# Kernel tuning notes

Hardware: AMD Instinct MI355X
Metric: run time of the kernel (lower is better)

The kernel has to match this reference:

```python
import jax, jax.numpy as jnp
import numpy as np

H = 2048          # hidden_size
NH = 32           # num_attention_heads
NKV = 8           # num_key_value_heads
HD = H // NH      # head_dim = 64
ROT = int(HD * 0.25)  # rotary_ndims = 16
THETA = 10000.0


def _rope_cos_sin(seq_len, position_ids):
    # inv_freq over the rotary dims
    inv_freq = 1.0 / (THETA ** (jnp.arange(0, ROT, 2, dtype=jnp.float32) / ROT))
    t = jnp.arange(seq_len, dtype=jnp.float32)
    freqs = jnp.outer(t, inv_freq)              # [S, ROT/2]
    emb = jnp.concatenate([freqs, freqs], -1)   # [S, ROT]
    cos = jnp.cos(emb)[position_ids][:, None]   # [B, 1, Q, ROT]
    sin = jnp.sin(emb)[position_ids][:, None]
    return cos, sin


def _rotate_half(x):
    x1, x2 = jnp.split(x, 2, axis=-1)
    return jnp.concatenate([-x2, x1], axis=-1)


def setup_inputs() -> dict:
    key = jax.random.key(0)
    ks = jax.random.split(key, 5)
    B, S = 2, 2048
    hidden_states = jax.random.normal(ks[0], (B, S, H), jnp.float32)
    # additive causal mask
    neg = jnp.finfo(jnp.float32).min
    causal = jnp.where(jnp.tril(jnp.ones((S, S), bool)), 0.0, neg).astype(jnp.float32)
    attention_mask = jnp.broadcast_to(causal[None, None], (B, 1, S, S))
    position_ids = jnp.broadcast_to(jnp.arange(S, dtype=jnp.int32)[None], (B, S))
    sc = 0.02
    Wq = jax.random.normal(ks[1], (H, H), jnp.float32) * sc
    Wk = jax.random.normal(ks[2], (NKV * HD, H), jnp.float32) * sc
    Wv = jax.random.normal(ks[3], (NKV * HD, H), jnp.float32) * sc
    Wo = jax.random.normal(ks[4], (H, H), jnp.float32) * sc
    return {"hidden_states": hidden_states, "attention_mask": attention_mask,
            "position_ids": position_ids, "Wq": Wq, "Wk": Wk, "Wv": Wv, "Wo": Wo}


def reference(hidden_states, attention_mask, position_ids, Wq, Wk, Wv, Wo):
    B, S, _ = hidden_states.shape
    q = (hidden_states @ Wq.T).reshape(B, S, NH, HD).transpose(0, 2, 1, 3)    # [B,NH,S,HD]
    k = (hidden_states @ Wk.T).reshape(B, S, NKV, HD).transpose(0, 2, 1, 3)   # [B,NKV,S,HD]
    v = (hidden_states @ Wv.T).reshape(B, S, NKV, HD).transpose(0, 2, 1, 3)

    cos, sin = _rope_cos_sin(S, position_ids)  # [B,1,S,ROT]
    q_rot, q_pass = q[..., :ROT], q[..., ROT:]
    k_rot, k_pass = k[..., :ROT], k[..., ROT:]
    q_rot = q_rot * cos + _rotate_half(q_rot) * sin
    k_rot = k_rot * cos + _rotate_half(k_rot) * sin
    q = jnp.concatenate([q_rot, q_pass], -1)
    k = jnp.concatenate([k_rot, k_pass], -1)

    # GQA without materializing repeated K/V: group Q heads per KV head
    G = NH // NKV
    qg = q.reshape(B, NKV, G, S, HD)
    scores = jnp.einsum('bhgqd,bhkd->bhgqk', qg, k) / np.sqrt(HD)
    scores = scores.reshape(B, NH, S, S) + attention_mask
    probs = jax.nn.softmax(scores.astype(jnp.float32), axis=-1).astype(q.dtype)
    out = jnp.einsum('bhgqk,bhkd->bhgqd', probs.reshape(B, NKV, G, S, S), v)
    out = out.reshape(B, NH, S, HD).transpose(0, 2, 1, 3).reshape(B, S, H)
    return out @ Wo.T
```

## Files before the change

kernel.cpp:

```cpp
#include <hip/hip_runtime.h>

typedef unsigned short u16;
typedef short s16x8 __attribute__((ext_vector_type(8)));
typedef u16 u16x8 __attribute__((ext_vector_type(8)));
typedef float f32x4 __attribute__((ext_vector_type(4)));
typedef __bf16 bf16x8 __attribute__((ext_vector_type(8)));

#define B_ 2
#define S_ 2048
#define H_ 2048
#define NH_ 32
#define NKV_ 8
#define HD_ 64
#define LDQ_ 3072
#define NTOK (B_ * S_)

__device__ __forceinline__ u16 f2bf(float f) {
  unsigned u = __float_as_uint(f);
  u += 0x7fffu + ((u >> 16) & 1u);
  return (u16)(u >> 16);
}
__device__ __forceinline__ float bf2f(u16 h) {
  return __uint_as_float(((unsigned)h) << 16);
}

__device__ __forceinline__ void gload16(const void* g, void* l) {
  __builtin_amdgcn_global_load_lds(
      (const __attribute__((address_space(1))) unsigned int*)g,
      (__attribute__((address_space(3))) unsigned int*)l, 16, 0, 0);
}

__device__ __forceinline__ f32x4 mfma16(s16x8 a, s16x8 b, f32x4 c) {
  return __builtin_amdgcn_mfma_f32_16x16x32_bf16(
      __builtin_bit_cast(bf16x8, a), __builtin_bit_cast(bf16x8, b), c, 0, 0, 0);
}

__global__ __launch_bounds__(256) void cvt_all(const float* __restrict__ hs,
    const float* __restrict__ wq, const float* __restrict__ wk,
    const float* __restrict__ wv, const float* __restrict__ wo,
    u16* __restrict__ xbf, u16* __restrict__ wqkv, u16* __restrict__ wob) {
  int i = blockIdx.x * 256 + threadIdx.x;
  const float* s; u16* d; int j;
  if (i < 1048576)      { s = hs; d = xbf;            j = i; }
  else if (i < 1572864) { s = wq; d = wqkv;           j = i - 1048576; }
  else if (i < 1703936) { s = wk; d = wqkv + 4194304; j = i - 1572864; }
  else if (i < 1835008) { s = wv; d = wqkv + 5242880; j = i - 1703936; }
  else                  { s = wo; d = wob;            j = i - 1835008; }
  const float4* sp = (const float4*)s + (size_t)j * 2;
  float4 a = sp[0], b = sp[1];
  u16x8 o;
  o[0] = f2bf(a.x); o[1] = f2bf(a.y); o[2] = f2bf(a.z); o[3] = f2bf(a.w);
  o[4] = f2bf(b.x); o[5] = f2bf(b.y); o[6] = f2bf(b.z); o[7] = f2bf(b.w);
  *((u16x8*)d + j) = o;
}

__global__ __launch_bounds__(256) void rope_table(float* __restrict__ tab) {
  int i = blockIdx.x * 256 + threadIdx.x;
  if (i >= S_ * 8) return;
  int p = i >> 3, k = i & 7;
  float inv = powf(10000.0f, -(float)k * 0.125f);
  float ang = (float)p * inv;
  tab[p * 16 + k] = cosf(ang);
  tab[p * 16 + 8 + k] = sinf(ang);
}

__global__ __launch_bounds__(256) void rope_apply(u16* __restrict__ C,
                                                  const int* __restrict__ pos,
                                                  const float* __restrict__ tab) {
  int t = blockIdx.x * 256 + threadIdx.x;
  if (t >= NTOK * 40) return;
  int token = t / 40, hh = t - token * 40;
  u16* p = C + (size_t)token * LDQ_ + (hh < 32 ? hh * 64 : 2048 + (hh - 32) * 64);
  const float* ct = tab + (size_t)pos[token] * 16;
  float x[16];
#pragma unroll
  for (int i = 0; i < 16; ++i) x[i] = bf2f(p[i]);
#pragma unroll
  for (int i = 0; i < 8; ++i) {
    float c = ct[i], s = ct[8 + i];
    p[i]     = f2bf(x[i] * c - x[i + 8] * s);
    p[i + 8] = f2bf(x[i + 8] * c + x[i] * s);
  }
}

__global__ __launch_bounds__(256) void vtrans(const u16* __restrict__ C,
                                              u16* __restrict__ Vt) {
  __shared__ u16 tile[64][72];
  int st = blockIdx.x;
  int kv = blockIdx.y;
  int tid = threadIdx.x;
  const u16* src = C + ((size_t)(kv >> 3) * S_ + (size_t)st * 64) * LDQ_ + 2560 + (kv & 7) * 64;
#pragma unroll
  for (int it = 0; it < 2; ++it) {
    int c = it * 256 + tid;
    int s = c >> 3, d0 = (c & 7) * 8;
    *(u16x8*)&tile[s][d0] = *(const u16x8*)(src + (size_t)s * LDQ_ + d0);
  }
  __syncthreads();
  u16* dst = Vt + (size_t)kv * HD_ * S_ + st * 64;
  int s = tid & 63;
#pragma unroll
  for (int it = 0; it < 16; ++it) {
    int d = it * 4 + (tid >> 6);
    dst[(size_t)d * S_ + s] = tile[s][d];
  }
}

__device__ __forceinline__ void store_c(u16* p, float v) { *p = f2bf(v); }
__device__ __forceinline__ void store_c(float* p, float v) { *p = v; }

template <typename OutT>
__global__ __launch_bounds__(256, 3) void gemm_bt(const u16* __restrict__ A,
                                                  const u16* __restrict__ Bw,
                                                  OutT* __restrict__ C,
                                                  int M, int N, int K) {
  __shared__ u16 lds[2 * 128 * 64];
  u16* ldsA = lds;
  u16* ldsB = lds + 128 * 64;
  const int tid = threadIdx.x;
  const int lane = tid & 63;
  const int wave = tid >> 6;
  const int wm = (wave & 1) * 64;
  const int wn = (wave >> 1) * 64;
  const int m0 = blockIdx.y * 128;
  const int n0 = blockIdx.x * 128;
  const int l15 = lane & 15;
  const int quad = lane >> 4;

  f32x4 acc[4][4];
#pragma unroll
  for (int i = 0; i < 4; ++i)
#pragma unroll
    for (int j = 0; j < 4; ++j) acc[i][j] = {0.f, 0.f, 0.f, 0.f};

  const u16* Ab = A + (size_t)m0 * K;
  const u16* Bb = Bw + (size_t)n0 * K;

  for (int k0 = 0; k0 < K; k0 += 64) {
    __syncthreads();
#pragma unroll
    for (int it = 0; it < 4; ++it) {
      int c = it * 256 + tid;
      int row = c >> 3;
      int kk = (c & 7) * 8;
      gload16(Ab + (size_t)row * K + k0 + kk, ldsA + (size_t)c * 8);
      gload16(Bb + (size_t)row * K + k0 + kk, ldsB + (size_t)c * 8);
    }
    __syncthreads();
#pragma unroll
    for (int ks = 0; ks < 2; ++ks) {
      int ko = ks * 32 + quad * 8;
      s16x8 af[4], bfr[4];
#pragma unroll
      for (int i = 0; i < 4; ++i)
        af[i] = *(const s16x8*)(ldsA + (size_t)(wm + i * 16 + l15) * 64 + ko);
#pragma unroll
      for (int j = 0; j < 4; ++j)
        bfr[j] = *(const s16x8*)(ldsB + (size_t)(wn + j * 16 + l15) * 64 + ko);
#pragma unroll
      for (int i = 0; i < 4; ++i)
#pragma unroll
        for (int j = 0; j < 4; ++j)
          acc[i][j] = mfma16(af[i], bfr[j], acc[i][j]);
    }
  }
#pragma unroll
  for (int i = 0; i < 4; ++i) {
    int row = m0 + wm + i * 16 + quad * 4;
#pragma unroll
    for (int j = 0; j < 4; ++j) {
      int col = n0 + wn + j * 16 + l15;
#pragma unroll
      for (int r = 0; r < 4; ++r) store_c(C + (size_t)(row + r) * N + col, acc[i][j][r]);
    }
  }
}

#define KSTRIDE 72
#define PSTRIDE 72
#define SC_ 0.18033688011112042f
#define M0_ 4.0f

template <bool DIAG>
__device__ __forceinline__ void softmax_pack(const f32x4* sc, f32x4& lacc,
                                             u16* pwq, int sb, int qg) {
#pragma unroll
  for (int nt = 0; nt < 4; ++nt) {
    f32x4 p;
#pragma unroll
    for (int r = 0; r < 4; ++r) {
      float v = fmaf(sc[nt][r], SC_, -M0_);
      float e = __builtin_amdgcn_exp2f(v);
      if (DIAG) e = (sb + nt * 16 + r > qg) ? 0.0f : e;
      p[r] = e;
    }
    lacc += p;
    unsigned lo = __builtin_amdgcn_perm(__float_as_uint(p[1]) + 0x8000u,
                                        __float_as_uint(p[0]) + 0x8000u,
                                        0x07060302u);
    unsigned hi = __builtin_amdgcn_perm(__float_as_uint(p[3]) + 0x8000u,
                                        __float_as_uint(p[2]) + 0x8000u,
                                        0x07060302u);
    *(unsigned*)(pwq + nt * 16) = lo;
    *(unsigned*)(pwq + nt * 16 + 2) = hi;
  }
}

__global__ __launch_bounds__(256, 3) void flash_attn(const u16* __restrict__ QKV,
                                                     const u16* __restrict__ Vt,
                                                     u16* __restrict__ O) {
  __shared__ u16 Kl2[2][64 * KSTRIDE];
  __shared__ u16 Vl2[2][64 * KSTRIDE];
  __shared__ u16 Pb[4][16 * PSTRIDE];
  const int h = blockIdx.x;
  const int b = blockIdx.y;
  const int qt = 15 - (int)blockIdx.z;
  const int kvh = h >> 2;
  const int tid = threadIdx.x;
  const int lane = tid & 63;
  const int wave = tid >> 6;
  const int l15 = lane & 15;
  const int quad = lane >> 4;

  const u16* Qb = QKV + (size_t)b * S_ * LDQ_ + h * 64;
  const u16* Kb = QKV + (size_t)b * S_ * LDQ_ + 2048 + kvh * 64;
  const u16* Vb = Vt + (size_t)(b * 8 + kvh) * HD_ * S_;

  const int row0w = qt * 128 + wave * 32;

  s16x8 qf[2][2];
#pragma unroll
  for (int g = 0; g < 2; ++g) {
    int qrow = row0w + g * 16 + l15;
#pragma unroll
    for (int ks = 0; ks < 2; ++ks)
      qf[g][ks] = *(const s16x8*)(Qb + (size_t)qrow * LDQ_ + ks * 32 + quad * 8);
  }

  f32x4 acc_o[2][4];
#pragma unroll
  for (int g = 0; g < 2; ++g)
#pragma unroll
    for (int nt = 0; nt < 4; ++nt) acc_o[g][nt] = {0.f, 0.f, 0.f, 0.f};
  f32x4 lacc[2] = {{0.f, 0.f, 0.f, 0.f}, {0.f, 0.f, 0.f, 0.f}};

  const int r0 = tid >> 3, ch0 = (tid & 7) * 8;
  const int r1 = r0 + 32, ch1 = ch0;

  const int nkt = 2 * qt + 2;

  u16* Pwq = Pb[wave] + l15 * PSTRIDE + quad * 4;
  const u16* Pr = Pb[wave] + l15 * PSTRIDE + quad * 8;

  u16x8 kr0, kr1, vr0, vr1;
  kr0 = *(const u16x8*)(Kb + (size_t)r0 * LDQ_ + ch0);
  kr1 = *(const u16x8*)(Kb + (size_t)r1 * LDQ_ + ch1);
  vr0 = *(const u16x8*)(Vb + (size_t)r0 * S_ + ch0);
  vr1 = *(const u16x8*)(Vb + (size_t)r1 * S_ + ch1);

  for (int kt = 0; kt < nkt; ++kt) {
    u16* Kl = Kl2[kt & 1];
    u16* Vl = Vl2[kt & 1];
    *(u16x8*)(Kl + r0 * KSTRIDE + ch0) = kr0;
    *(u16x8*)(Kl + r1 * KSTRIDE + ch1) = kr1;
    *(u16x8*)(Vl + r0 * KSTRIDE + ch0) = vr0;
    *(u16x8*)(Vl + r1 * KSTRIDE + ch1) = vr1;
    __syncthreads();
    if (kt + 1 < nkt) {
      int kb = (kt + 1) * 64;
      kr0 = *(const u16x8*)(Kb + (size_t)(kb + r0) * LDQ_ + ch0);
      kr1 = *(const u16x8*)(Kb + (size_t)(kb + r1) * LDQ_ + ch1);
      vr0 = *(const u16x8*)(Vb + (size_t)r0 * S_ + kb + ch0);
      vr1 = *(const u16x8*)(Vb + (size_t)r1 * S_ + kb + ch1);
    }
    if (kt * 64 <= row0w + 31) {
      f32x4 sc[2][4];
#pragma unroll
      for (int nt = 0; nt < 4; ++nt) {
        const u16* kp = Kl + (nt * 16 + l15) * KSTRIDE + quad * 8;
        s16x8 k0 = *(const s16x8*)(kp);
        s16x8 k1 = *(const s16x8*)(kp + 32);
        f32x4 z = {0.f, 0.f, 0.f, 0.f};
        sc[0][nt] = mfma16(k1, qf[0][1], mfma16(k0, qf[0][0], z));
        sc[1][nt] = mfma16(k1, qf[1][1], mfma16(k0, qf[1][0], z));
      }
      const int sb = kt * 64 + quad * 4;
      s16x8 pf[2][2];
#pragma unroll
      for (int g = 0; g < 2; ++g) {
        const int row0 = row0w + g * 16;
        if (kt * 64 + 63 > row0)
          softmax_pack<true>(sc[g], lacc[g], Pwq, sb, row0 + l15);
        else
          softmax_pack<false>(sc[g], lacc[g], Pwq, sb, row0 + l15);
        pf[g][0] = *(const s16x8*)(Pr);
        pf[g][1] = *(const s16x8*)(Pr + 32);
      }
#pragma unroll
      for (int nt = 0; nt < 4; ++nt) {
        const u16* vp = Vl + (nt * 16 + l15) * KSTRIDE + quad * 8;
        s16x8 v0 = *(const s16x8*)(vp);
        s16x8 v1 = *(const s16x8*)(vp + 32);
        acc_o[0][nt] = mfma16(pf[0][1], v1, mfma16(pf[0][0], v0, acc_o[0][nt]));
        acc_o[1][nt] = mfma16(pf[1][1], v1, mfma16(pf[1][0], v0, acc_o[1][nt]));
      }
    }
  }
#pragma unroll
  for (int g = 0; g < 2; ++g) {
    float l = (lacc[g][0] + lacc[g][1]) + (lacc[g][2] + lacc[g][3]);
    l += __shfl_xor(l, 16);
    l += __shfl_xor(l, 32);
#pragma unroll
    for (int r = 0; r < 4; ++r) {
      float ls = __shfl(l, quad * 4 + r);
      float inv = 1.0f / ls;
      int row = row0w + g * 16 + quad * 4 + r;
      size_t obase = ((size_t)b * S_ + row) * (size_t)H_ + h * 64;
#pragma unroll
      for (int nt = 0; nt < 4; ++nt)
        O[obase + nt * 16 + l15] = f2bf(acc_o[g][nt][r] * inv);
    }
  }
}

extern "C" void kernel_launch(void* const* d_in, const int* in_sizes, int n_in,
                              void* d_out, int out_size, void* d_ws, size_t ws_size,
                              hipStream_t stream) {
  const float* hs = (const float*)d_in[0];
  const int* pos = (const int*)d_in[2];
  const float* Wq = (const float*)d_in[3];
  const float* Wk = (const float*)d_in[4];
  const float* Wv = (const float*)d_in[5];
  const float* Wo = (const float*)d_in[6];
  float* out = (float*)d_out;

  if (ws_size < 67239936) return;

  char* ws = (char*)d_ws;
  u16* Xbf   = (u16*)(ws);
  u16* Wqkv  = (u16*)(ws + 16777216);
  u16* Wob   = (u16*)(ws + 29360128);
  u16* Cqkv  = (u16*)(ws + 37748736);
  u16* Vt    = (u16*)(ws + 62914560);
  float* tab = (float*)(ws + 67108864);
  u16* O     = Xbf;

  cvt_all<<<9216, 256, 0, stream>>>(hs, Wq, Wk, Wv, Wo, Xbf, Wqkv, Wob);
  rope_table<<<64, 256, 0, stream>>>(tab);

  gemm_bt<u16><<<dim3(24, 32), 256, 0, stream>>>(Xbf, Wqkv, Cqkv, 4096, 3072, 2048);
  rope_apply<<<640, 256, 0, stream>>>(Cqkv, pos, tab);
  vtrans<<<dim3(32, 16), 256, 0, stream>>>(Cqkv, Vt);
  flash_attn<<<dim3(32, 2, 16), 256, 0, stream>>>(Cqkv, Vt, O);
  gemm_bt<float><<<dim3(16, 32), 256, 0, stream>>>(O, Wob, out, 4096, 2048, 2048);
}
```

Measured before the change: 312.1 us.

## XOR-swizzle GEMM LDS tiles and merge small rope/convert/transpose launches

The GEMM's LDS staging now places each 16-byte chunk at an XOR-swizzled slot keyed on row, and the MFMA fragment reads use the same swizzle. This is meant to remove bank conflicts on the row-strided fragment loads. Separately, the rope table build is folded into the convert kernel, and rope application plus the V transpose are merged into one launch, cutting two kernel launches. Rope and V-transpose touch disjoint columns, so running them in one grid should be safe.

```diff
diff --git a/kernel.cpp b/kernel.cpp
--- a/kernel.cpp
+++ b/kernel.cpp
@@ -38,8 +38,20 @@
 __global__ __launch_bounds__(256) void cvt_all(const float* __restrict__ hs,
     const float* __restrict__ wq, const float* __restrict__ wk,
     const float* __restrict__ wv, const float* __restrict__ wo,
-    u16* __restrict__ xbf, u16* __restrict__ wqkv, u16* __restrict__ wob) {
+    u16* __restrict__ xbf, u16* __restrict__ wqkv, u16* __restrict__ wob,
+    float* __restrict__ tab) {
   int i = blockIdx.x * 256 + threadIdx.x;
+  if (i >= 2359296) {
+    int t = i - 2359296;
+    if (t < S_ * 8) {
+      int p = t >> 3, k = t & 7;
+      float inv = powf(10000.0f, -(float)k * 0.125f);
+      float ang = (float)p * inv;
+      tab[p * 16 + k] = cosf(ang);
+      tab[p * 16 + 8 + k] = sinf(ang);
+    }
+    return;
+  }
   const float* s; u16* d; int j;
   if (i < 1048576)      { s = hs; d = xbf;            j = i; }
   else if (i < 1572864) { s = wq; d = wqkv;           j = i - 1048576; }
@@ -54,41 +66,32 @@
   *((u16x8*)d + j) = o;
 }
 
-__global__ __launch_bounds__(256) void rope_table(float* __restrict__ tab) {
-  int i = blockIdx.x * 256 + threadIdx.x;
-  if (i >= S_ * 8) return;
-  int p = i >> 3, k = i & 7;
-  float inv = powf(10000.0f, -(float)k * 0.125f);
-  float ang = (float)p * inv;
-  tab[p * 16 + k] = cosf(ang);
-  tab[p * 16 + 8 + k] = sinf(ang);
-}
-
-__global__ __launch_bounds__(256) void rope_apply(u16* __restrict__ C,
-                                                  const int* __restrict__ pos,
-                                                  const float* __restrict__ tab) {
-  int t = blockIdx.x * 256 + threadIdx.x;
-  if (t >= NTOK * 40) return;
-  int token = t / 40, hh = t - token * 40;
-  u16* p = C + (size_t)token * LDQ_ + (hh < 32 ? hh * 64 : 2048 + (hh - 32) * 64);
-  const float* ct = tab + (size_t)pos[token] * 16;
-  float x[16];
-#pragma unroll
-  for (int i = 0; i < 16; ++i) x[i] = bf2f(p[i]);
-#pragma unroll
-  for (int i = 0; i < 8; ++i) {
-    float c = ct[i], s = ct[8 + i];
-    p[i]     = f2bf(x[i] * c - x[i + 8] * s);
-    p[i + 8] = f2bf(x[i + 8] * c + x[i] * s);
-  }
-}
-
-__global__ __launch_bounds__(256) void vtrans(const u16* __restrict__ C,
-                                              u16* __restrict__ Vt) {
+__global__ __launch_bounds__(256) void rope_vtrans(u16* __restrict__ C,
+                                                   const int* __restrict__ pos,
+                                                   const float* __restrict__ tab,
+                                                   u16* __restrict__ Vt) {
   __shared__ u16 tile[64][72];
-  int st = blockIdx.x;
-  int kv = blockIdx.y;
+  int bid = blockIdx.x;
   int tid = threadIdx.x;
+  if (bid < 640) {
+    int t = bid * 256 + tid;
+    int token = t / 40, hh = t - token * 40;
+    u16* p = C + (size_t)token * LDQ_ + (hh < 32 ? hh * 64 : 2048 + (hh - 32) * 64);
+    const float* ct = tab + (size_t)pos[token] * 16;
+    float x[16];
+#pragma unroll
+    for (int i = 0; i < 16; ++i) x[i] = bf2f(p[i]);
+#pragma unroll
+    for (int i = 0; i < 8; ++i) {
+      float c = ct[i], s = ct[8 + i];
+      p[i]     = f2bf(x[i] * c - x[i + 8] * s);
+      p[i + 8] = f2bf(x[i + 8] * c + x[i] * s);
+    }
+    return;
+  }
+  int b2 = bid - 640;
+  int st = b2 & 31;
+  int kv = b2 >> 5;
   const u16* src = C + ((size_t)(kv >> 3) * S_ + (size_t)st * 64) * LDQ_ + 2560 + (kv & 7) * 64;
 #pragma unroll
   for (int it = 0; it < 2; ++it) {
@@ -126,6 +129,7 @@
   const int n0 = blockIdx.x * 128;
   const int l15 = lane & 15;
   const int quad = lane >> 4;
+  const int xs = l15 & 7;
 
   f32x4 acc[4][4];
 #pragma unroll
@@ -142,21 +146,21 @@
     for (int it = 0; it < 4; ++it) {
       int c = it * 256 + tid;
       int row = c >> 3;
-      int kk = (c & 7) * 8;
-      gload16(Ab + (size_t)row * K + k0 + kk, ldsA + (size_t)c * 8);
-      gload16(Bb + (size_t)row * K + k0 + kk, ldsB + (size_t)c * 8);
+      int sw = ((c & 7) ^ (row & 7)) * 8;
+      gload16(Ab + (size_t)row * K + k0 + sw, ldsA + (size_t)c * 8);
+      gload16(Bb + (size_t)row * K + k0 + sw, ldsB + (size_t)c * 8);
     }
     __syncthreads();
 #pragma unroll
     for (int ks = 0; ks < 2; ++ks) {
-      int ko = ks * 32 + quad * 8;
+      int slot = ((ks * 4 + quad) ^ xs) * 8;
       s16x8 af[4], bfr[4];
 #pragma unroll
       for (int i = 0; i < 4; ++i)
-        af[i] = *(const s16x8*)(ldsA + (size_t)(wm + i * 16 + l15) * 64 + ko);
+        af[i] = *(const s16x8*)(ldsA + (size_t)(wm + i * 16 + l15) * 64 + slot);
 #pragma unroll
       for (int j = 0; j < 4; ++j)
-        bfr[j] = *(const s16x8*)(ldsB + (size_t)(wn + j * 16 + l15) * 64 + ko);
+        bfr[j] = *(const s16x8*)(ldsB + (size_t)(wn + j * 16 + l15) * 64 + slot);
 #pragma unroll
       for (int i = 0; i < 4; ++i)
 #pragma unroll
@@ -346,12 +350,9 @@
   float* tab = (float*)(ws + 67108864);
   u16* O     = Xbf;
 
-  cvt_all<<<9216, 256, 0, stream>>>(hs, Wq, Wk, Wv, Wo, Xbf, Wqkv, Wob);
-  rope_table<<<64, 256, 0, stream>>>(tab);
-
+  cvt_all<<<9280, 256, 0, stream>>>(hs, Wq, Wk, Wv, Wo, Xbf, Wqkv, Wob, tab);
   gemm_bt<u16><<<dim3(24, 32), 256, 0, stream>>>(Xbf, Wqkv, Cqkv, 4096, 3072, 2048);
-  rope_apply<<<640, 256, 0, stream>>>(Cqkv, pos, tab);
-  vtrans<<<dim3(32, 16), 256, 0, stream>>>(Cqkv, Vt);
+  rope_vtrans<<<1152, 256, 0, stream>>>(Cqkv, pos, tab, Vt);
   flash_attn<<<dim3(32, 2, 16), 256, 0, stream>>>(Cqkv, Vt, O);
   gemm_bt<float><<<dim3(16, 32), 256, 0, stream>>>(O, Wob, out, 4096, 2048, 2048);
 }
```

New measurement: 291.4 us. -6.6%, faster.
